# Kernel tuning notes

Measured on AMD Instinct MI355X. Metric: run time of the kernel, lower is better.

The kernel has to match this reference:

```python
import jax, jax.numpy as jnp
import numpy as np

B, S, D, H = 2, 2048, 1024, 16
HD = D // H  # head_dim = 64


def setup_inputs() -> dict:
    key = jax.random.key(0)
    ks = jax.random.split(key, 9)
    s_in = 1.0 / np.sqrt(D)
    inp = {
        "hidden_state": jax.random.normal(ks[0], (B, S, D), dtype=jnp.float32),
        # per-head projections, stacked: [H, D, HD]
        "Wq": jax.random.uniform(ks[1], (H, D, HD), jnp.float32, -s_in, s_in),
        "bq": jax.random.uniform(ks[2], (H, HD), jnp.float32, -s_in, s_in),
        "Wk": jax.random.uniform(ks[3], (H, D, HD), jnp.float32, -s_in, s_in),
        "bk": jax.random.uniform(ks[4], (H, HD), jnp.float32, -s_in, s_in),
        "Wv": jax.random.uniform(ks[5], (H, D, HD), jnp.float32, -s_in, s_in),
        "bv": jax.random.uniform(ks[6], (H, HD), jnp.float32, -s_in, s_in),
        # output linear: [D, D]
        "Wo": jax.random.uniform(ks[7], (D, D), jnp.float32, -s_in, s_in),
        "bo": jax.random.uniform(ks[8], (D,), jnp.float32, -s_in, s_in),
    }
    return inp


def reference(hidden_state, Wq, bq, Wk, bk, Wv, bv, Wo, bo):
    # fused per-head projections: [B, H, S, HD]
    q = jnp.einsum("bsd,hde->bhse", hidden_state, Wq) + bq[None, :, None, :]
    k = jnp.einsum("bsd,hde->bhse", hidden_state, Wk) + bk[None, :, None, :]
    v = jnp.einsum("bsd,hde->bhse", hidden_state, Wv) + bv[None, :, None, :]
    scale = 1.0 / jnp.sqrt(jnp.float32(HD))
    scores = jnp.einsum("bhse,bhte->bhst", q, k) * scale  # [B, H, S, S]
    weights = jax.nn.softmax(scores, axis=-1)
    ctx = jnp.einsum("bhst,bhte->bhse", weights, v)       # [B, H, S, HD]
    # concat heads along last dim -> [B, S, D]
    ctx = jnp.transpose(ctx, (0, 2, 1, 3)).reshape(B, S, D)
    return ctx @ Wo + bo
```

## Files before the change

kernel.cpp:

```cpp
#include <hip/hip_runtime.h>
#include <hip/hip_bf16.h>
#include <math.h>

#define BB 2
#define SS 2048
#define DD 1024
#define HH 16
#define HD 64

typedef __attribute__((ext_vector_type(8))) _Float16 f16x8;
typedef __attribute__((ext_vector_type(2))) __fp16 fp16x2;
typedef __attribute__((ext_vector_type(8))) unsigned short u16x8;
typedef __attribute__((ext_vector_type(4))) float f32x4;
typedef __attribute__((ext_vector_type(4))) unsigned short u16x4;

__device__ __forceinline__ unsigned short hbits(_Float16 h) {
    union { _Float16 h; unsigned short s; } u; u.h = h; return u.s;
}

__device__ __forceinline__ int swz(int row, int grp) {
    return (row << 6) + (((grp) ^ (row & 7)) << 3);
}

__device__ __forceinline__ float fexp2(float x) {
#if __has_builtin(__builtin_amdgcn_exp2f)
    return __builtin_amdgcn_exp2f(x);
#else
    return exp2f(x);
#endif
}

__device__ __forceinline__ u16x4 pack4(float p0, float p1, float p2, float p3) {
#if __has_builtin(__builtin_amdgcn_cvt_pkrtz)
    union { fp16x2 h[2]; u16x4 u; } pu;
    pu.h[0] = __builtin_amdgcn_cvt_pkrtz(p0, p1);
    pu.h[1] = __builtin_amdgcn_cvt_pkrtz(p2, p3);
    return pu.u;
#else
    u16x4 r;
    r[0] = hbits((_Float16)p0); r[1] = hbits((_Float16)p1);
    r[2] = hbits((_Float16)p2); r[3] = hbits((_Float16)p3);
    return r;
#endif
}

__device__ __forceinline__ void gload_lds16(const unsigned short* g, unsigned short* l) {
#if __has_builtin(__builtin_amdgcn_global_load_lds)
    auto gp = (const __attribute__((address_space(1))) unsigned int*)(uintptr_t)g;
    auto lp = (__attribute__((address_space(3))) unsigned int*)(uintptr_t)l;
    __builtin_amdgcn_global_load_lds(gp, lp, 16, 0, 0);
#else
    *(u16x8*)(l + (threadIdx.x & 63) * 8) = *(const u16x8*)g;
#endif
}

__global__ __launch_bounds__(256) void prep_convert(
    const float* __restrict__ X,
    const float* __restrict__ Wq, const float* __restrict__ Wk,
    const float* __restrict__ Wv, const float* __restrict__ Wo,
    unsigned short* __restrict__ Xh, unsigned short* __restrict__ WT)
{
    __shared__ __align__(16) unsigned short LT[64 * 68];
    const int bid = blockIdx.x;
    const int tid = threadIdx.x;

    if (bid < 2048) {
        const int base = bid * 2048 + tid * 8;
        float4 a = *(const float4*)&X[base];
        float4 b = *(const float4*)&X[base + 4];
        u16x8 o;
        o[0] = hbits((_Float16)a.x); o[1] = hbits((_Float16)a.y);
        o[2] = hbits((_Float16)a.z); o[3] = hbits((_Float16)a.w);
        o[4] = hbits((_Float16)b.x); o[5] = hbits((_Float16)b.y);
        o[6] = hbits((_Float16)b.z); o[7] = hbits((_Float16)b.w);
        *(u16x8*)&Xh[base] = o;
        return;
    }

    const int t = bid - 2048;
    const float* src;
    size_t stride;
    int outRow0, kcol0;
    if (t < 768) {
        const int nt = t >> 4, ktile = t & 15;
        const int sel = nt >> 4, hh = nt & 15;
        const float* Ws = (sel == 0) ? Wq : ((sel == 1) ? Wk : Wv);
        src = Ws + (size_t)hh * (DD * HD) + (size_t)ktile * 64 * HD;
        stride = HD;
        outRow0 = nt * 64;
        kcol0 = ktile * 64;
    } else {
        const int tt = t - 768;
        const int nt = tt & 15, ktile = tt >> 4;
        src = Wo + (size_t)ktile * 64 * DD + nt * 64;
        stride = DD;
        outRow0 = 3072 + nt * 64;
        kcol0 = ktile * 64;
    }

    const int e = tid & 63, dq = tid >> 6;
#pragma unroll
    for (int p = 0; p < 16; p++) {
        const int dl = p * 4 + dq;
        LT[e * 68 + dl] = hbits((_Float16)src[(size_t)dl * stride + e]);
    }
    __syncthreads();
    const int eo = tid >> 2, d16 = (tid & 3) * 16;
#pragma unroll
    for (int j = 0; j < 4; j++) {
        *(ushort4*)&WT[(size_t)(outRow0 + eo) * DD + kcol0 + d16 + j * 4] =
            *(const ushort4*)&LT[eo * 68 + d16 + j * 4];
    }
}

__global__ __launch_bounds__(256) void vtrans(
    const unsigned short* __restrict__ vh, unsigned short* __restrict__ vTs)
{
    __shared__ __align__(16) unsigned short LT[64 * 72];
    const int bh = blockIdx.x >> 5;
    const int tile = blockIdx.x & 31;
    const int tid = threadIdx.x;
    const unsigned short* src = vh + (size_t)bh * SS * HD + (size_t)tile * 64 * HD;
    unsigned short* dst = vTs + (size_t)bh * SS * HD + (size_t)tile * 4096;

#pragma unroll
    for (int p = 0; p < 2; p++) {
        const int idx8 = p * 256 + tid;
        const int key = idx8 >> 3, d8 = (idx8 & 7) * 8;
        *(u16x8*)&LT[key * 72 + d8] = *(const u16x8*)&src[key * HD + d8];
    }
    __syncthreads();
#pragma unroll
    for (int p = 0; p < 2; p++) {
        const int o8 = p * 256 + tid;
        const int e = o8 >> 3, q8 = o8 & 7;
        const int g = q8 ^ (e & 7);
        u16x8 v;
#pragma unroll
        for (int j = 0; j < 8; j++)
            v[j] = LT[(g * 8 + j) * 72 + e];
        *(u16x8*)&dst[o8 * 8] = v;
    }
}

#define GBM 128
#define GBN 128
#define GBK 64

__global__ __launch_bounds__(256) void qkv_gemm(
    const unsigned short* __restrict__ Xh, const unsigned short* __restrict__ WT,
    const float* __restrict__ bq, const float* __restrict__ bk,
    const float* __restrict__ bv,
    unsigned short* __restrict__ qh, unsigned short* __restrict__ kh,
    unsigned short* __restrict__ vh, unsigned int* __restrict__ kc2)
{
    __shared__ __align__(16) unsigned short As[16 * 512];
    __shared__ __align__(16) unsigned short Bs[16 * 512];

    const int tid = threadIdx.x;
    const int m0 = blockIdx.y * GBM;
    const int n0 = blockIdx.x * GBN;
    const int lane = tid & 63;
    const int w = tid >> 6;
    const int wm = w & 1, wn = w >> 1;
    const int l15 = lane & 15, quad = lane >> 4;

    int g_off[4];
#pragma unroll
    for (int p = 0; p < 4; p++) {
        const int c = p * 4 + w;
        g_off[p] = ((c >> 1) * 16 + (lane & 15)) * DD + (c & 1) * 32 + (lane >> 4) * 8;
    }

    f32x4 acc[4][4];
#pragma unroll
    for (int i = 0; i < 4; i++)
#pragma unroll
        for (int j = 0; j < 4; j++) acc[i][j] = (f32x4){0.f, 0.f, 0.f, 0.f};

    const unsigned short* Abase = Xh + (size_t)m0 * DD;
    const unsigned short* Bbase = WT + (size_t)n0 * DD;

    for (int kt = 0; kt < DD; kt += GBK) {
        __syncthreads();
#pragma unroll
        for (int p = 0; p < 4; p++) {
            gload_lds16(Abase + g_off[p] + kt, &As[(p * 4 + w) * 512]);
            gload_lds16(Bbase + g_off[p] + kt, &Bs[(p * 4 + w) * 512]);
        }
        __syncthreads();
#pragma unroll
        for (int ks = 0; ks < 2; ks++) {
            f16x8 af[4], bf[4];
#pragma unroll
            for (int i = 0; i < 4; i++) {
                af[i] = *(const f16x8*)&As[((wm * 4 + i) * 2 + ks) * 512 + lane * 8];
                bf[i] = *(const f16x8*)&Bs[((wn * 4 + i) * 2 + ks) * 512 + lane * 8];
            }
#pragma unroll
            for (int ns = 0; ns < 4; ns++)
#pragma unroll
                for (int ms = 0; ms < 4; ms++)
                    acc[ms][ns] = __builtin_amdgcn_mfma_f32_16x16x32_f16(
                        af[ms], bf[ns], acc[ms][ns], 0, 0, 0);
        }
    }

    const int sel = n0 >> 10;
    const int hw = ((n0 + wn * 64) >> 6) & 15;
    const int bblk = m0 >> 11;
    const float* bias = (sel == 0) ? bq : ((sel == 1) ? bk : bv);
    const size_t bh_base = ((size_t)bblk * HH + hw) * SS * HD;
    float wmx = 0.0f;
#pragma unroll
    for (int ms = 0; ms < 4; ms++) {
#pragma unroll
        for (int rr = 0; rr < 4; rr++) {
            const int m = m0 + wm * 64 + ms * 16 + quad * 4 + rr;
            const int s = m & (SS - 1);
            float v2 = 0.0f;
#pragma unroll
            for (int ns = 0; ns < 4; ns++) {
                const int e = ns * 16 + l15;
                const float val = acc[ms][ns][rr] + bias[hw * HD + e];
                if (sel == 0) {
                    qh[bh_base + (size_t)s * HD + e] = hbits((_Float16)val);
                } else if (sel == 1) {
                    v2 = fmaf(val, val, v2);
                    const size_t kofs = bh_base + (size_t)(s >> 6) * 4096
                                      + swz(s & 63, e >> 3) + (e & 7);
                    kh[kofs] = hbits((_Float16)val);
                } else {
                    vh[bh_base + (size_t)s * HD + e] = hbits((_Float16)val);
                }
            }
            if (sel == 1) {
                v2 += __shfl_xor(v2, 1);
                v2 += __shfl_xor(v2, 2);
                v2 += __shfl_xor(v2, 4);
                v2 += __shfl_xor(v2, 8);
                wmx = fmaxf(wmx, v2);
            }
        }
    }
    if (sel == 1) {
        wmx = fmaxf(wmx, __shfl_xor(wmx, 16));
        wmx = fmaxf(wmx, __shfl_xor(wmx, 32));
        if (lane == 0)
            atomicMax(&kc2[bblk * HH + hw], __float_as_uint(wmx));
    }
}

__global__ __launch_bounds__(256) void out_gemm(
    const unsigned short* __restrict__ Ctxh, const unsigned short* __restrict__ WoT,
    const float* __restrict__ bo, float* __restrict__ out)
{
    __shared__ __align__(16) unsigned short As[16 * 512];
    __shared__ __align__(16) unsigned short Bs[16 * 512];

    const int tid = threadIdx.x;
    const int m0 = blockIdx.y * GBM;
    const int n0 = blockIdx.x * GBN;
    const int lane = tid & 63;
    const int w = tid >> 6;
    const int wm = w & 1, wn = w >> 1;
    const int l15 = lane & 15, quad = lane >> 4;

    int g_off[4];
#pragma unroll
    for (int p = 0; p < 4; p++) {
        const int c = p * 4 + w;
        g_off[p] = ((c >> 1) * 16 + (lane & 15)) * DD + (c & 1) * 32 + (lane >> 4) * 8;
    }

    f32x4 acc[4][4];
#pragma unroll
    for (int i = 0; i < 4; i++)
#pragma unroll
        for (int j = 0; j < 4; j++) acc[i][j] = (f32x4){0.f, 0.f, 0.f, 0.f};

    const unsigned short* Abase = Ctxh + (size_t)m0 * DD;
    const unsigned short* Bbase = WoT + (size_t)n0 * DD;

    for (int kt = 0; kt < DD; kt += GBK) {
        __syncthreads();
#pragma unroll
        for (int p = 0; p < 4; p++) {
            gload_lds16(Abase + g_off[p] + kt, &As[(p * 4 + w) * 512]);
            gload_lds16(Bbase + g_off[p] + kt, &Bs[(p * 4 + w) * 512]);
        }
        __syncthreads();
#pragma unroll
        for (int ks = 0; ks < 2; ks++) {
            f16x8 af[4], bf[4];
#pragma unroll
            for (int i = 0; i < 4; i++) {
                af[i] = *(const f16x8*)&As[((wm * 4 + i) * 2 + ks) * 512 + lane * 8];
                bf[i] = *(const f16x8*)&Bs[((wn * 4 + i) * 2 + ks) * 512 + lane * 8];
            }
#pragma unroll
            for (int ns = 0; ns < 4; ns++)
#pragma unroll
                for (int ms = 0; ms < 4; ms++)
                    acc[ms][ns] = __builtin_amdgcn_mfma_f32_16x16x32_f16(
                        af[ms], bf[ns], acc[ms][ns], 0, 0, 0);
        }
    }

#pragma unroll
    for (int ms = 0; ms < 4; ms++) {
#pragma unroll
        for (int rr = 0; rr < 4; rr++) {
            const size_t m = (size_t)(m0 + wm * 64 + ms * 16 + quad * 4 + rr);
#pragma unroll
            for (int ns = 0; ns < 4; ns++) {
                const int n = n0 + wn * 64 + ns * 16 + l15;
                out[m * DD + n] = acc[ms][ns][rr] + bo[n];
            }
        }
    }
}

#define TQB 128
#define TKB 64
#define C1 0.1803368801111204f

__global__ __launch_bounds__(256) void attn_mfma(
    const unsigned short* __restrict__ qh, const unsigned short* __restrict__ kh,
    const unsigned short* __restrict__ vTs, const unsigned int* __restrict__ kc2,
    unsigned short* __restrict__ ctxh)
{
    __shared__ __align__(16) unsigned short KL [TKB * 64];
    __shared__ __align__(16) unsigned short VtL[HD * 64];
    __shared__ __align__(16) unsigned short PsL[4][32 * 64];

    const int tid  = threadIdx.x;
    const int lane = tid & 63;
    const int w    = tid >> 6;
    const int l15  = lane & 15;
    const int quad = lane >> 4;
    const int bh   = blockIdx.y;
    const int q0   = blockIdx.x * TQB;

    const float kfac = sqrtf(__uint_as_float(kc2[bh])) * 1.01f * C1;

    f16x8 qf[2][2];
    float M2[2];
#pragma unroll
    for (int msub = 0; msub < 2; msub++) {
        const unsigned short* qrow =
            qh + ((size_t)bh * SS + q0 + w * 32 + msub * 16 + l15) * HD;
        float nq2 = 0.0f;
#pragma unroll
        for (int dstep = 0; dstep < 2; dstep++) {
            qf[msub][dstep] = *(const f16x8*)&qrow[dstep * 32 + quad * 8];
#pragma unroll
            for (int j = 0; j < 8; j++) {
                const float x = (float)qf[msub][dstep][j];
                nq2 = fmaf(x, x, nq2);
            }
        }
        nq2 += __shfl_xor(nq2, 16);
        nq2 += __shfl_xor(nq2, 32);
        M2[msub] = sqrtf(nq2) * kfac;
    }

    f16x8 ones;
#pragma unroll
    for (int j = 0; j < 8; j++) ones[j] = (_Float16)1.0f;

    f32x4 o[2][4], lones[2];
#pragma unroll
    for (int ms = 0; ms < 2; ms++) {
        lones[ms] = (f32x4){0.f, 0.f, 0.f, 0.f};
#pragma unroll
        for (int e = 0; e < 4; e++) o[ms][e] = (f32x4){0.f, 0.f, 0.f, 0.f};
    }

    const unsigned short* kb0 = kh  + (size_t)bh * SS * HD;
    const unsigned short* vb0 = vTs + (size_t)bh * SS * HD;

    for (int t = 0; t < SS / TKB; t++) {
        __syncthreads();

        const unsigned short* kb = kb0 + (size_t)t * 4096;
        const unsigned short* vb = vb0 + (size_t)t * 4096;
        gload_lds16(kb + tid * 8,        &KL [w * 512]);
        gload_lds16(kb + 2048 + tid * 8, &KL [2048 + w * 512]);
        gload_lds16(vb + tid * 8,        &VtL[w * 512]);
        gload_lds16(vb + 2048 + tid * 8, &VtL[2048 + w * 512]);
        __syncthreads();

        f32x4 sc[2][4];
#pragma unroll
        for (int ksub = 0; ksub < 4; ksub++) {
            const int row = ksub * 16 + l15;
            f16x8 k0 = *(const f16x8*)&KL[swz(row, quad)];
            f16x8 k1 = *(const f16x8*)&KL[swz(row, 4 + quad)];
#pragma unroll
            for (int msub = 0; msub < 2; msub++) {
                f32x4 a = (f32x4){0.f, 0.f, 0.f, 0.f};
                a = __builtin_amdgcn_mfma_f32_16x16x32_f16(k0, qf[msub][0], a, 0, 0, 0);
                a = __builtin_amdgcn_mfma_f32_16x16x32_f16(k1, qf[msub][1], a, 0, 0, 0);
                sc[msub][ksub] = a;
            }
        }

#pragma unroll
        for (int msub = 0; msub < 2; msub++) {
            const int prow = msub * 16 + l15;
#pragma unroll
            for (int ksub = 0; ksub < 4; ksub++) {
                const float p0 = fexp2(fmaf(sc[msub][ksub][0], C1, -M2[msub]));
                const float p1 = fexp2(fmaf(sc[msub][ksub][1], C1, -M2[msub]));
                const float p2 = fexp2(fmaf(sc[msub][ksub][2], C1, -M2[msub]));
                const float p3 = fexp2(fmaf(sc[msub][ksub][3], C1, -M2[msub]));
                *(u16x4*)&PsL[w][swz(prow, ksub * 2 + (quad >> 1)) + (quad & 1) * 4] =
                    pack4(p0, p1, p2, p3);
            }
        }

#pragma unroll
        for (int kj = 0; kj < 2; kj++) {
            f16x8 pa[2];
#pragma unroll
            for (int msub = 0; msub < 2; msub++)
                pa[msub] = *(const f16x8*)&PsL[w][swz(msub * 16 + l15, kj * 4 + quad)];
            lones[0] = __builtin_amdgcn_mfma_f32_16x16x32_f16(pa[0], ones, lones[0], 0, 0, 0);
            lones[1] = __builtin_amdgcn_mfma_f32_16x16x32_f16(pa[1], ones, lones[1], 0, 0, 0);
#pragma unroll
            for (int esub = 0; esub < 4; esub++) {
                f16x8 vr = *(const f16x8*)&VtL[swz(esub * 16 + l15, kj * 4 + quad)];
                o[0][esub] = __builtin_amdgcn_mfma_f32_16x16x32_f16(pa[0], vr, o[0][esub], 0, 0, 0);
                o[1][esub] = __builtin_amdgcn_mfma_f32_16x16x32_f16(pa[1], vr, o[1][esub], 0, 0, 0);
            }
        }
    }

    const int b = bh >> 4;
    const int h = bh & 15;
#pragma unroll
    for (int msub = 0; msub < 2; msub++) {
#pragma unroll
        for (int rr = 0; rr < 4; rr++) {
            const float linv = 1.0f / lones[msub][rr];
            const int row = q0 + w * 32 + msub * 16 + quad * 4 + rr;
#pragma unroll
            for (int esub = 0; esub < 4; esub++) {
                ctxh[((size_t)b * SS + row) * DD + h * HD + esub * 16 + l15] =
                    hbits((_Float16)(o[msub][esub][rr] * linv));
            }
        }
    }
}

extern "C" void kernel_launch(void* const* d_in, const int* in_sizes, int n_in,
                              void* d_out, int out_size, void* d_ws, size_t ws_size,
                              hipStream_t stream) {
    const float* X  = (const float*)d_in[0];
    const float* Wq = (const float*)d_in[1];
    const float* bq = (const float*)d_in[2];
    const float* Wk = (const float*)d_in[3];
    const float* bk = (const float*)d_in[4];
    const float* Wv = (const float*)d_in[5];
    const float* bv = (const float*)d_in[6];
    const float* Wo = (const float*)d_in[7];
    const float* bo = (const float*)d_in[8];
    float* out = (float*)d_out;

    const size_t NB2 = (size_t)4096 * 1024 * 2;
    unsigned char* w8 = (unsigned char*)d_ws;
    unsigned short* Xh   = (unsigned short*)(w8);
    unsigned short* WT   = (unsigned short*)(w8 + NB2);
    unsigned short* qh   = (unsigned short*)(w8 + 2 * NB2);
    unsigned short* kh   = (unsigned short*)(w8 + 3 * NB2);
    unsigned short* vh   = (unsigned short*)(w8 + 4 * NB2);
    unsigned short* vTs  = (unsigned short*)(w8 + 5 * NB2);
    unsigned short* ctxh = (unsigned short*)(w8 + 6 * NB2);
    unsigned int*   kc2  = (unsigned int*)(w8 + 7 * NB2);
    unsigned short* WoT  = WT + (size_t)3072 * 1024;

    (void)hipMemsetAsync(kc2, 0, BB * HH * sizeof(unsigned int), stream);

    prep_convert<<<dim3(3072), 256, 0, stream>>>(X, Wq, Wk, Wv, Wo, Xh, WT);

    qkv_gemm<<<dim3(3072 / GBN, 4096 / GBM), 256, 0, stream>>>(
        Xh, WT, bq, bk, bv, qh, kh, vh, kc2);

    vtrans<<<dim3(BB * HH * 32), 256, 0, stream>>>(vh, vTs);

    attn_mfma<<<dim3(SS / TQB, BB * HH), 256, 0, stream>>>(qh, kh, vTs, kc2, ctxh);

    out_gemm<<<dim3(1024 / GBN, 4096 / GBM), 256, 0, stream>>>(ctxh, WoT, bo, out);
}
```

Baseline: 241.3 us.

## Double-buffer LDS tiles in GEMMs and attention; fuse V transpose into QKV epilogue

Each GEMM and the attention kernel now uses two LDS buffers and prefetches the next K-step tile while computing on the current one. This drops one barrier per iteration and hides global-to-LDS latency. The V projection epilogue writes straight into the swizzled transposed layout that attention reads, so the separate vtrans kernel and its extra round trip through global memory go away. The cost is doubled LDS use, which may lower occupancy, plus scattered 2-byte stores in the V epilogue.

```diff
diff --git a/kernel.cpp b/kernel.cpp
--- a/kernel.cpp
+++ b/kernel.cpp
@@ -113,49 +113,20 @@
     }
 }
 
-__global__ __launch_bounds__(256) void vtrans(
-    const unsigned short* __restrict__ vh, unsigned short* __restrict__ vTs)
-{
-    __shared__ __align__(16) unsigned short LT[64 * 72];
-    const int bh = blockIdx.x >> 5;
-    const int tile = blockIdx.x & 31;
-    const int tid = threadIdx.x;
-    const unsigned short* src = vh + (size_t)bh * SS * HD + (size_t)tile * 64 * HD;
-    unsigned short* dst = vTs + (size_t)bh * SS * HD + (size_t)tile * 4096;
-
-#pragma unroll
-    for (int p = 0; p < 2; p++) {
-        const int idx8 = p * 256 + tid;
-        const int key = idx8 >> 3, d8 = (idx8 & 7) * 8;
-        *(u16x8*)&LT[key * 72 + d8] = *(const u16x8*)&src[key * HD + d8];
-    }
-    __syncthreads();
-#pragma unroll
-    for (int p = 0; p < 2; p++) {
-        const int o8 = p * 256 + tid;
-        const int e = o8 >> 3, q8 = o8 & 7;
-        const int g = q8 ^ (e & 7);
-        u16x8 v;
-#pragma unroll
-        for (int j = 0; j < 8; j++)
-            v[j] = LT[(g * 8 + j) * 72 + e];
-        *(u16x8*)&dst[o8 * 8] = v;
-    }
-}
-
 #define GBM 128
 #define GBN 128
 #define GBK 64
+#define NKT (DD / GBK)
 
 __global__ __launch_bounds__(256) void qkv_gemm(
     const unsigned short* __restrict__ Xh, const unsigned short* __restrict__ WT,
     const float* __restrict__ bq, const float* __restrict__ bk,
     const float* __restrict__ bv,
     unsigned short* __restrict__ qh, unsigned short* __restrict__ kh,
-    unsigned short* __restrict__ vh, unsigned int* __restrict__ kc2)
+    unsigned short* __restrict__ vTs, unsigned int* __restrict__ kc2)
 {
-    __shared__ __align__(16) unsigned short As[16 * 512];
-    __shared__ __align__(16) unsigned short Bs[16 * 512];
+    __shared__ __align__(16) unsigned short As[2][16 * 512];
+    __shared__ __align__(16) unsigned short Bs[2][16 * 512];
 
     const int tid = threadIdx.x;
     const int m0 = blockIdx.y * GBM;
@@ -181,21 +152,30 @@
     const unsigned short* Abase = Xh + (size_t)m0 * DD;
     const unsigned short* Bbase = WT + (size_t)n0 * DD;
 
-    for (int kt = 0; kt < DD; kt += GBK) {
+#pragma unroll
+    for (int p = 0; p < 4; p++) {
+        gload_lds16(Abase + g_off[p], &As[0][(p * 4 + w) * 512]);
+        gload_lds16(Bbase + g_off[p], &Bs[0][(p * 4 + w) * 512]);
+    }
+
+    for (int it = 0; it < NKT; it++) {
+        const int cur = it & 1;
         __syncthreads();
-#pragma unroll
-        for (int p = 0; p < 4; p++) {
-            gload_lds16(Abase + g_off[p] + kt, &As[(p * 4 + w) * 512]);
-            gload_lds16(Bbase + g_off[p] + kt, &Bs[(p * 4 + w) * 512]);
-        }
-        __syncthreads();
+        if (it + 1 < NKT) {
+            const int kt2 = (it + 1) * GBK;
+#pragma unroll
+            for (int p = 0; p < 4; p++) {
+                gload_lds16(Abase + g_off[p] + kt2, &As[cur ^ 1][(p * 4 + w) * 512]);
+                gload_lds16(Bbase + g_off[p] + kt2, &Bs[cur ^ 1][(p * 4 + w) * 512]);
+            }
+        }
 #pragma unroll
         for (int ks = 0; ks < 2; ks++) {
             f16x8 af[4], bf[4];
 #pragma unroll
             for (int i = 0; i < 4; i++) {
-                af[i] = *(const f16x8*)&As[((wm * 4 + i) * 2 + ks) * 512 + lane * 8];
-                bf[i] = *(const f16x8*)&Bs[((wn * 4 + i) * 2 + ks) * 512 + lane * 8];
+                af[i] = *(const f16x8*)&As[cur][((wm * 4 + i) * 2 + ks) * 512 + lane * 8];
+                bf[i] = *(const f16x8*)&Bs[cur][((wn * 4 + i) * 2 + ks) * 512 + lane * 8];
             }
 #pragma unroll
             for (int ns = 0; ns < 4; ns++)
@@ -218,6 +198,7 @@
         for (int rr = 0; rr < 4; rr++) {
             const int m = m0 + wm * 64 + ms * 16 + quad * 4 + rr;
             const int s = m & (SS - 1);
+            const int s63 = s & 63;
             float v2 = 0.0f;
 #pragma unroll
             for (int ns = 0; ns < 4; ns++) {
@@ -228,10 +209,12 @@
                 } else if (sel == 1) {
                     v2 = fmaf(val, val, v2);
                     const size_t kofs = bh_base + (size_t)(s >> 6) * 4096
-                                      + swz(s & 63, e >> 3) + (e & 7);
+                                      + swz(s63, e >> 3) + (e & 7);
                     kh[kofs] = hbits((_Float16)val);
                 } else {
-                    vh[bh_base + (size_t)s * HD + e] = hbits((_Float16)val);
+                    const size_t vofs = bh_base + (size_t)(s >> 6) * 4096
+                                      + swz(e, s63 >> 3) + (s63 & 7);
+                    vTs[vofs] = hbits((_Float16)val);
                 }
             }
             if (sel == 1) {
@@ -255,8 +238,8 @@
     const unsigned short* __restrict__ Ctxh, const unsigned short* __restrict__ WoT,
     const float* __restrict__ bo, float* __restrict__ out)
 {
-    __shared__ __align__(16) unsigned short As[16 * 512];
-    __shared__ __align__(16) unsigned short Bs[16 * 512];
+    __shared__ __align__(16) unsigned short As[2][16 * 512];
+    __shared__ __align__(16) unsigned short Bs[2][16 * 512];
 
     const int tid = threadIdx.x;
     const int m0 = blockIdx.y * GBM;
@@ -282,21 +265,30 @@
     const unsigned short* Abase = Ctxh + (size_t)m0 * DD;
     const unsigned short* Bbase = WoT + (size_t)n0 * DD;
 
-    for (int kt = 0; kt < DD; kt += GBK) {
+#pragma unroll
+    for (int p = 0; p < 4; p++) {
+        gload_lds16(Abase + g_off[p], &As[0][(p * 4 + w) * 512]);
+        gload_lds16(Bbase + g_off[p], &Bs[0][(p * 4 + w) * 512]);
+    }
+
+    for (int it = 0; it < NKT; it++) {
+        const int cur = it & 1;
         __syncthreads();
-#pragma unroll
-        for (int p = 0; p < 4; p++) {
-            gload_lds16(Abase + g_off[p] + kt, &As[(p * 4 + w) * 512]);
-            gload_lds16(Bbase + g_off[p] + kt, &Bs[(p * 4 + w) * 512]);
-        }
-        __syncthreads();
+        if (it + 1 < NKT) {
+            const int kt2 = (it + 1) * GBK;
+#pragma unroll
+            for (int p = 0; p < 4; p++) {
+                gload_lds16(Abase + g_off[p] + kt2, &As[cur ^ 1][(p * 4 + w) * 512]);
+                gload_lds16(Bbase + g_off[p] + kt2, &Bs[cur ^ 1][(p * 4 + w) * 512]);
+            }
+        }
 #pragma unroll
         for (int ks = 0; ks < 2; ks++) {
             f16x8 af[4], bf[4];
 #pragma unroll
             for (int i = 0; i < 4; i++) {
-                af[i] = *(const f16x8*)&As[((wm * 4 + i) * 2 + ks) * 512 + lane * 8];
-                bf[i] = *(const f16x8*)&Bs[((wn * 4 + i) * 2 + ks) * 512 + lane * 8];
+                af[i] = *(const f16x8*)&As[cur][((wm * 4 + i) * 2 + ks) * 512 + lane * 8];
+                bf[i] = *(const f16x8*)&Bs[cur][((wn * 4 + i) * 2 + ks) * 512 + lane * 8];
             }
 #pragma unroll
             for (int ns = 0; ns < 4; ns++)
@@ -323,6 +315,7 @@
 
 #define TQB 128
 #define TKB 64
+#define NT (SS / TKB)
 #define C1 0.1803368801111204f
 
 __global__ __launch_bounds__(256) void attn_mfma(
@@ -330,8 +323,8 @@
     const unsigned short* __restrict__ vTs, const unsigned int* __restrict__ kc2,
     unsigned short* __restrict__ ctxh)
 {
-    __shared__ __align__(16) unsigned short KL [TKB * 64];
-    __shared__ __align__(16) unsigned short VtL[HD * 64];
+    __shared__ __align__(16) unsigned short KL [2][TKB * 64];
+    __shared__ __align__(16) unsigned short VtL[2][HD * 64];
     __shared__ __align__(16) unsigned short PsL[4][32 * 64];
 
     const int tid  = threadIdx.x;
@@ -380,23 +373,29 @@
     const unsigned short* kb0 = kh  + (size_t)bh * SS * HD;
     const unsigned short* vb0 = vTs + (size_t)bh * SS * HD;
 
-    for (int t = 0; t < SS / TKB; t++) {
+    gload_lds16(kb0 + tid * 8,        &KL [0][w * 512]);
+    gload_lds16(kb0 + 2048 + tid * 8, &KL [0][2048 + w * 512]);
+    gload_lds16(vb0 + tid * 8,        &VtL[0][w * 512]);
+    gload_lds16(vb0 + 2048 + tid * 8, &VtL[0][2048 + w * 512]);
+
+    for (int t = 0; t < NT; t++) {
+        const int cur = t & 1;
         __syncthreads();
-
-        const unsigned short* kb = kb0 + (size_t)t * 4096;
-        const unsigned short* vb = vb0 + (size_t)t * 4096;
-        gload_lds16(kb + tid * 8,        &KL [w * 512]);
-        gload_lds16(kb + 2048 + tid * 8, &KL [2048 + w * 512]);
-        gload_lds16(vb + tid * 8,        &VtL[w * 512]);
-        gload_lds16(vb + 2048 + tid * 8, &VtL[2048 + w * 512]);
-        __syncthreads();
+        if (t + 1 < NT) {
+            const unsigned short* kb = kb0 + (size_t)(t + 1) * 4096;
+            const unsigned short* vb = vb0 + (size_t)(t + 1) * 4096;
+            gload_lds16(kb + tid * 8,        &KL [cur ^ 1][w * 512]);
+            gload_lds16(kb + 2048 + tid * 8, &KL [cur ^ 1][2048 + w * 512]);
+            gload_lds16(vb + tid * 8,        &VtL[cur ^ 1][w * 512]);
+            gload_lds16(vb + 2048 + tid * 8, &VtL[cur ^ 1][2048 + w * 512]);
+        }
 
         f32x4 sc[2][4];
 #pragma unroll
         for (int ksub = 0; ksub < 4; ksub++) {
             const int row = ksub * 16 + l15;
-            f16x8 k0 = *(const f16x8*)&KL[swz(row, quad)];
-            f16x8 k1 = *(const f16x8*)&KL[swz(row, 4 + quad)];
+            f16x8 k0 = *(const f16x8*)&KL[cur][swz(row, quad)];
+            f16x8 k1 = *(const f16x8*)&KL[cur][swz(row, 4 + quad)];
 #pragma unroll
             for (int msub = 0; msub < 2; msub++) {
                 f32x4 a = (f32x4){0.f, 0.f, 0.f, 0.f};
@@ -430,7 +429,7 @@
             lones[1] = __builtin_amdgcn_mfma_f32_16x16x32_f16(pa[1], ones, lones[1], 0, 0, 0);
 #pragma unroll
             for (int esub = 0; esub < 4; esub++) {
-                f16x8 vr = *(const f16x8*)&VtL[swz(esub * 16 + l15, kj * 4 + quad)];
+                f16x8 vr = *(const f16x8*)&VtL[cur][swz(esub * 16 + l15, kj * 4 + quad)];
                 o[0][esub] = __builtin_amdgcn_mfma_f32_16x16x32_f16(pa[0], vr, o[0][esub], 0, 0, 0);
                 o[1][esub] = __builtin_amdgcn_mfma_f32_16x16x32_f16(pa[1], vr, o[1][esub], 0, 0, 0);
             }
@@ -474,10 +473,9 @@
     unsigned short* WT   = (unsigned short*)(w8 + NB2);
     unsigned short* qh   = (unsigned short*)(w8 + 2 * NB2);
     unsigned short* kh   = (unsigned short*)(w8 + 3 * NB2);
-    unsigned short* vh   = (unsigned short*)(w8 + 4 * NB2);
-    unsigned short* vTs  = (unsigned short*)(w8 + 5 * NB2);
-    unsigned short* ctxh = (unsigned short*)(w8 + 6 * NB2);
-    unsigned int*   kc2  = (unsigned int*)(w8 + 7 * NB2);
+    unsigned short* vTs  = (unsigned short*)(w8 + 4 * NB2);
+    unsigned short* ctxh = (unsigned short*)(w8 + 5 * NB2);
+    unsigned int*   kc2  = (unsigned int*)(w8 + 6 * NB2);
     unsigned short* WoT  = WT + (size_t)3072 * 1024;
 
     (void)hipMemsetAsync(kc2, 0, BB * HH * sizeof(unsigned int), stream);
@@ -485,9 +483,7 @@
     prep_convert<<<dim3(3072), 256, 0, stream>>>(X, Wq, Wk, Wv, Wo, Xh, WT);
 
     qkv_gemm<<<dim3(3072 / GBN, 4096 / GBM), 256, 0, stream>>>(
-        Xh, WT, bq, bk, bv, qh, kh, vh, kc2);
-
-    vtrans<<<dim3(BB * HH * 32), 256, 0, stream>>>(vh, vTs);
+        Xh, WT, bq, bk, bv, qh, kh, vTs, kc2);
 
     attn_mfma<<<dim3(SS / TQB, BB * HH), 256, 0, stream>>>(qh, kh, vTs, kc2, ctxh);
 
```

Result: faster. 235.5 us (-2.4%).
